# Kernel tuning notes

Measured on AMD Instinct MI355X. Metric: run time of the kernel, lower is better.

## Reference

```python
import jax, jax.numpy as jnp
import numpy as np

SIGMA1 = 1.0        # RBF bandwidth for kernel1
DYADIC_ORDER = 1    # dyadic grid refinement
LAMBD = 1.0         # ridge regularizer
INPUT_SCALE = 0.1   # keep signature-kernel values in fp32 range


def rbf_gram(X, Y, sigma):
    # X: (N,S,D), Y: (M,T,D) -> (N,M,S,T), sigkernel RBFKernel: exp(-||x-y||^2 / sigma)
    x2 = jnp.sum(X * X, axis=-1)  # (N,S)
    y2 = jnp.sum(Y * Y, axis=-1)  # (M,T)
    xy = jnp.einsum('nsd,mtd->nmst', X, Y)
    d2 = x2[:, None, :, None] + y2[None, :, None, :] - 2.0 * xy
    return jnp.exp(-d2 / sigma)


def linear_gram(X, Y):
    # sigkernel LinearKernel: inner product Gram
    return jnp.einsum('nsd,mtd->nmst', X, Y)


def sig_kernel_gram(G, dyadic_order):
    """Solve the Goursat PDE for the signature kernel on a dyadic grid.

    G: (N,M,S,T) static-kernel Gram. Returns (N,M) signature-kernel Gram.
    Update (sigkernel explicit scheme):
      k[i+1,j+1] = (k[i+1,j] + k[i,j+1]) * (1 + inc/2 + inc^2/12)
                   - k[i,j] * (1 - inc^2/12)
    """
    N, M, S, T = G.shape
    # double increments of the static kernel
    inc = G[:, :, 1:, 1:] - G[:, :, 1:, :-1] - G[:, :, :-1, 1:] + G[:, :, :-1, :-1]
    f = 2 ** dyadic_order
    inc = jnp.repeat(jnp.repeat(inc, f, axis=2), f, axis=3) / float(f * f)
    B = N * M
    P, Q = (S - 1) * f, (T - 1) * f
    inc = inc.reshape(B, P, Q)
    C1 = 1.0 + 0.5 * inc + inc * inc * (1.0 / 12.0)
    C2 = 1.0 - inc * inc * (1.0 / 12.0)
    ones_b = jnp.ones((B,), G.dtype)

    def row_step(prev_row, coeffs):
        c1, c2 = coeffs  # (B,Q) each

        def col_step(left, v):
            c1j, c2j, pj, pjm1 = v  # each (B,)
            new = (left + pj) * c1j - pjm1 * c2j
            return new, new

        xs = (c1.T, c2.T, prev_row[:, 1:].T, prev_row[:, :-1].T)  # (Q,B)
        _, vals = jax.lax.scan(col_step, ones_b, xs)  # (Q,B)
        new_row = jnp.concatenate([ones_b[:, None], vals.T], axis=1)  # (B,Q+1)
        return new_row, None

    row0 = jnp.ones((B, Q + 1), G.dtype)
    last_row, _ = jax.lax.scan(row_step, row0, (jnp.moveaxis(C1, 1, 0), jnp.moveaxis(C2, 1, 0)))
    return last_row[:, -1].reshape(N, M)


def cmmd(x, y, z):
    N = x.shape[0]
    K = sig_kernel_gram(rbf_gram(x, x, SIGMA1), DYADIC_ORDER)
    L_gen = sig_kernel_gram(linear_gram(y, y), DYADIC_ORDER)
    L_true = sig_kernel_gram(linear_gram(z, z), DYADIC_ORDER)
    L_mix = sig_kernel_gram(linear_gram(y, z), DYADIC_ORDER)
    Ktildeinv = jnp.linalg.inv(K + jnp.eye(N, dtype=K.dtype) * LAMBD)
    A = K @ Ktildeinv  # shared left factor

    def tr(L):
        return jnp.trace(A @ (L @ Ktildeinv))

    return tr(L_gen) + tr(L_true) - 2.0 * tr(L_mix)


def setup_inputs() -> dict:
    key = jax.random.key(0)
    k1, k2, k3 = jax.random.split(key, 3)
    shape = (64, 33, 8)
    return {
        'x': jax.random.normal(k1, shape, dtype=jnp.float32) * INPUT_SCALE,
        'y': jax.random.normal(k2, shape, dtype=jnp.float32) * INPUT_SCALE,
        'z': jax.random.normal(k3, shape, dtype=jnp.float32) * INPUT_SCALE,
    }


def reference(x, y, z):
    return cmmd(x, y, z)
```

## Files before the change

### kernel.cpp

```cpp
#include <hip/hip_runtime.h>
#include <hip/hip_fp16.h>
#include <math.h>


#define SLEN 33

__device__ __forceinline__ float rl(float v, int lane) {
    return __int_as_float(__builtin_amdgcn_readlane(__float_as_int(v), lane));
}

__global__ __launch_bounds__(64, 5)
void sigker_pde_kernel(const float* __restrict__ x,
                       const float* __restrict__ y,
                       const float* __restrict__ z,
                       float* __restrict__ ws) {
    __shared__ float4 Xi4[2][66];
    __shared__ __half incH[2][1024];

    const int lane = threadIdx.x;
    const int h = lane >> 5;
    const int p = lane & 31;

    int b = blockIdx.x, g, loc;
    if (b < 1040)      { g = 0; loc = b; }
    else if (b < 2080) { g = 1; loc = b - 1040; }
    else if (b < 3120) { g = 2; loc = b - 2080; }
    else               { g = 3; loc = b - 3120; }

    int pair = 2 * loc + h, gi, gj;
    if (g == 3) {
        gi = pair >> 6; gj = pair & 63;
    } else {
        float ff = sqrtf(8.0f * (float)pair + 1.0f);
        gi = (int)((ff - 1.0f) * 0.5f);
        while ((gi + 1) * (gi + 2) / 2 <= pair) ++gi;
        while (gi * (gi + 1) / 2 > pair) --gi;
        gj = pair - gi * (gi + 1) / 2;
    }

    const float* Ap = (g == 0) ? x : ((g == 2) ? z : y);
    const float* Bp = (g == 0) ? x : ((g == 1) ? y : z);
    const float4* As = (const float4*)(Ap + gi * (SLEN * 8));
    const float4* Bs = (const float4*)(Bp + gj * (SLEN * 8));

    for (int k = p; k < 66; k += 32) Xi4[h][k] = As[k];
    float4 b0 = Bs[2*p],   b1 = Bs[2*p+1];
    float4 b2 = Bs[2*p+2], b3 = Bs[2*p+3];
    __syncthreads();

    if (g == 0) {
        float nprev;
        {
            float4 a0 = Xi4[h][0], a1 = Xi4[h][1];
            float d0=a0.x-b0.x,d1=a0.y-b0.y,d2=a0.z-b0.z,d3=a0.w-b0.w;
            float d4=a1.x-b1.x,d5=a1.y-b1.y,d6=a1.z-b1.z,d7=a1.w-b1.w;
            float da = d0*d0+d1*d1+d2*d2+d3*d3+d4*d4+d5*d5+d6*d6+d7*d7;
            float e0=a0.x-b2.x,e1=a0.y-b2.y,e2=a0.z-b2.z,e3=a0.w-b2.w;
            float e4=a1.x-b3.x,e5=a1.y-b3.y,e6=a1.z-b3.z,e7=a1.w-b3.w;
            float db = e0*e0+e1*e1+e2*e2+e3*e3+e4*e4+e5*e5+e6*e6+e7*e7;
            nprev = __expf(-db) - __expf(-da);
        }
        for (int k = 1; k <= 32; ++k) {
            float4 a0 = Xi4[h][2*k], a1 = Xi4[h][2*k+1];
            float d0=a0.x-b0.x,d1=a0.y-b0.y,d2=a0.z-b0.z,d3=a0.w-b0.w;
            float d4=a1.x-b1.x,d5=a1.y-b1.y,d6=a1.z-b1.z,d7=a1.w-b1.w;
            float da = d0*d0+d1*d1+d2*d2+d3*d3+d4*d4+d5*d5+d6*d6+d7*d7;
            float e0=a0.x-b2.x,e1=a0.y-b2.y,e2=a0.z-b2.z,e3=a0.w-b2.w;
            float e4=a1.x-b3.x,e5=a1.y-b3.y,e6=a1.z-b3.z,e7=a1.w-b3.w;
            float db = e0*e0+e1*e1+e2*e2+e3*e3+e4*e4+e5*e5+e6*e6+e7*e7;
            float diffk = __expf(-db) - __expf(-da);
            incH[h][(k-1)*32 + p] = __float2half(0.25f * (diffk - nprev));
            nprev = diffk;
        }
    } else {
        float e0=b2.x-b0.x, e1=b2.y-b0.y, e2=b2.z-b0.z, e3=b2.w-b0.w;
        float e4=b3.x-b1.x, e5=b3.y-b1.y, e6=b3.z-b1.z, e7=b3.w-b1.w;
        float4 a0 = Xi4[h][0], a1 = Xi4[h][1];
        #pragma unroll 4
        for (int k = 0; k < 32; ++k) {
            float4 a2 = Xi4[h][2*k+2], a3 = Xi4[h][2*k+3];
            float acc = (a2.x-a0.x)*e0 + (a2.y-a0.y)*e1
                      + (a2.z-a0.z)*e2 + (a2.w-a0.w)*e3
                      + (a3.x-a1.x)*e4 + (a3.y-a1.y)*e5
                      + (a3.z-a1.z)*e6 + (a3.w-a1.w)*e7;
            incH[h][k*32 + p] = __float2half(0.25f * acc);
            a0 = a2; a1 = a3;
        }
    }
    __syncthreads();

    float c01 = 1.0f, c10 = 1.0f, c11 = 1.0f, dcarry = 1.0f;
    const bool isrow0 = (p == 0);
    const __half* incrow = &incH[h][p * 32];
    #pragma unroll 4
    for (int m = 0; m < 63; ++m) {
        float nb10 = __shfl_up(c10, 1);
        float nb11 = __shfl_up(c11, 1);
        int t = m - p;
        float incv = __half2float(incrow[t & 31]);
        float n0 = isrow0 ? 1.0f : nb10;
        float n1 = isrow0 ? 1.0f : nb11;
        bool t0 = (t == 0);
        float w0 = t0 ? 1.0f : c01;
        float w1 = t0 ? 1.0f : c11;
        float d  = t0 ? 1.0f : dcarry;
        float i2 = incv * incv * (1.0f / 12.0f);
        float C1 = 1.0f + 0.5f * incv + i2;
        float C2 = 1.0f - i2;
        float v00 = (w0  + n0 ) * C1 - d   * C2;
        float v01 = (v00 + n1 ) * C1 - n0  * C2;
        float v10 = (v00 + w1 ) * C1 - w0  * C2;
        float v11 = (v10 + v01) * C1 - v00 * C2;
        c01 = v01; c10 = v10; c11 = v11;
        dcarry = n1;
    }

    if (p == 31) {
        float* dst = ws + g * 4096;
        dst[gi * 64 + gj] = c11;
        if (g != 3) dst[gj * 64 + gi] = c11;
    }
}

__global__ __launch_bounds__(1024, 1)
void gj_trace_kernel(const float* __restrict__ ws, float* __restrict__ out) {
    __shared__ float prow[2][2][64];
    __shared__ float Kls[64 * 65];
    __shared__ float red[16];

    const int tid = threadIdx.x;
    const int c = tid & 63, w = tid >> 6;
    const float* K  = ws;
    const float* Lg = ws + 4096;
    const float* Lt = ws + 8192;
    const float* Lm = ws + 12288;

    float m[4];
    #pragma unroll
    for (int i = 0; i < 4; ++i) {
        int r = w * 4 + i;
        m[i] = K[r * 64 + c] + ((r == c) ? 1.0f : 0.0f);
    }

    #pragma unroll
    for (int rnd = 0; rnd < 32; ++rnd) {
        const int p0 = 2 * rnd, p1 = p0 + 1;
        const int wp = p0 >> 2;
        const int i0 = p0 & 3, i1 = i0 + 1;
        const int buf = rnd & 1;
        if (w == wp) {
            float a  = rl(m[i0], p0), bq = rl(m[i0], p1);
            float cq = rl(m[i1], p0), dq = rl(m[i1], p1);
            float dinv = 1.0f / (a * dq - bq * cq);
            float P00 =  dq * dinv, P01 = -bq * dinv;
            float P10 = -cq * dinv, P11 =  a  * dinv;
            float sp0 = P00 * m[i0] + P01 * m[i1];
            float sp1 = P10 * m[i0] + P11 * m[i1];
            sp0 = (c == p0) ? P00 : ((c == p1) ? P01 : sp0);
            sp1 = (c == p0) ? P10 : ((c == p1) ? P11 : sp1);
            m[i0] = sp0; m[i1] = sp1;
            prow[buf][0][c] = sp0;
            prow[buf][1][c] = sp1;
        }
        __syncthreads();
        float s0 = prow[buf][0][c],  s1 = prow[buf][1][c];
        float q00 = prow[buf][0][p0], q01 = prow[buf][0][p1];
        float q10 = prow[buf][1][p0], q11 = prow[buf][1][p1];
        #pragma unroll
        for (int i = 0; i < 4; ++i) {
            bool pivotRow = (w == wp) && (i == i0 || i == i1);
            float f0 = rl(m[i], p0);
            float f1 = rl(m[i], p1);
            float nv = m[i] - f0 * s0 - f1 * s1;
            float wb0 = -(f0 * q00 + f1 * q10);
            float wb1 = -(f0 * q01 + f1 * q11);
            nv = (c == p0) ? wb0 : ((c == p1) ? wb1 : nv);
            if (!pivotRow) m[i] = nv;
        }
    }

    #pragma unroll
    for (int i = 0; i < 4; ++i)
        Kls[(w * 4 + i) * 65 + c] = m[i];
    __syncthreads();

    float acc[4] = {0.0f, 0.0f, 0.0f, 0.0f};
    #pragma unroll 4
    for (int k = 0; k < 64; ++k) {
        float rv = Kls[k * 65 + c];
        #pragma unroll
        for (int i = 0; i < 4; ++i)
            acc[i] = fmaf(rl(m[i], k), rv, acc[i]);
    }

    float local = 0.0f;
    #pragma unroll
    for (int i = 0; i < 4; ++i) {
        int r = w * 4 + i;
        float lc = Lg[r * 64 + c] + Lt[r * 64 + c] - 2.0f * Lm[r * 64 + c];
        local += (m[i] - acc[i]) * lc;
    }
    #pragma unroll
    for (int off = 32; off > 0; off >>= 1)
        local += __shfl_down(local, off);
    if (c == 0) red[w] = local;
    __syncthreads();
    if (tid == 0) {
        float v = 0.0f;
        #pragma unroll
        for (int i = 0; i < 16; ++i) v += red[i];
        out[0] = v;
    }
}

extern "C" void kernel_launch(void* const* d_in, const int* in_sizes, int n_in,
                              void* d_out, int out_size, void* d_ws, size_t ws_size,
                              hipStream_t stream) {
    const float* x = (const float*)d_in[0];
    const float* y = (const float*)d_in[1];
    const float* z = (const float*)d_in[2];
    float* out = (float*)d_out;
    float* ws  = (float*)d_ws;

    sigker_pde_kernel<<<5168, 64, 0, stream>>>(x, y, z, ws);
    gj_trace_kernel<<<1, 1024, 0, stream>>>(ws, out);
}
```

Before: 105.4 us.

## Map each lane to two PDE rows and pack four pairs per wavefront

The PDE kernel now gives each lane a 2-row strip of the 64x64 dyadic grid, so 16 lanes serve one pair and a 64-lane block handles four pairs. Increments are stored as packed half2 values, one per row pair. The wavefront sweep shortens from 63 to 47 steps, and the block count halves. The intent is to cut shuffle-serialized anti-diagonal steps and raise work per wave, at the cost of more registers (launch bounds lowered to 3) and a longer dependent chain per step. The Gauss-Jordan loop is also switched to a non-unrolled form with runtime row selection to shrink code size.

```diff
diff --git a/kernel.cpp b/kernel.cpp
--- a/kernel.cpp
+++ b/kernel.cpp
@@ -9,25 +9,25 @@
     return __int_as_float(__builtin_amdgcn_readlane(__float_as_int(v), lane));
 }
 
-__global__ __launch_bounds__(64, 5)
+__global__ __launch_bounds__(64, 3)
 void sigker_pde_kernel(const float* __restrict__ x,
                        const float* __restrict__ y,
                        const float* __restrict__ z,
                        float* __restrict__ ws) {
-    __shared__ float4 Xi4[2][66];
-    __shared__ __half incH[2][1024];
+    __shared__ float4 XiS[4][66];
+    __shared__ __half2 inc2[4 * 520];
 
     const int lane = threadIdx.x;
-    const int h = lane >> 5;
-    const int p = lane & 31;
+    const int qt = lane >> 4;
+    const int s  = lane & 15;
 
     int b = blockIdx.x, g, loc;
-    if (b < 1040)      { g = 0; loc = b; }
-    else if (b < 2080) { g = 1; loc = b - 1040; }
-    else if (b < 3120) { g = 2; loc = b - 2080; }
-    else               { g = 3; loc = b - 3120; }
-
-    int pair = 2 * loc + h, gi, gj;
+    if (b < 520)       { g = 0; loc = b; }
+    else if (b < 1040) { g = 1; loc = b - 520; }
+    else if (b < 1560) { g = 2; loc = b - 1040; }
+    else               { g = 3; loc = b - 1560; }
+
+    int pair = 4 * loc + qt, gi, gj;
     if (g == 3) {
         gi = pair >> 6; gj = pair & 63;
     } else {
@@ -43,82 +43,122 @@
     const float4* As = (const float4*)(Ap + gi * (SLEN * 8));
     const float4* Bs = (const float4*)(Bp + gj * (SLEN * 8));
 
-    for (int k = p; k < 66; k += 32) Xi4[h][k] = As[k];
-    float4 b0 = Bs[2*p],   b1 = Bs[2*p+1];
-    float4 b2 = Bs[2*p+2], b3 = Bs[2*p+3];
-    __syncthreads();
+    for (int k = s; k < 66; k += 16) XiS[qt][k] = As[k];
+    float4 q0 = Bs[4*s],   q1 = Bs[4*s+1], q2 = Bs[4*s+2],
+           q3 = Bs[4*s+3], q4 = Bs[4*s+4], q5 = Bs[4*s+5];
+    __syncthreads();
+
+    __half2* incw = inc2 + qt * 520;
 
     if (g == 0) {
-        float nprev;
+        float p0g, p1g, p2g;
         {
-            float4 a0 = Xi4[h][0], a1 = Xi4[h][1];
-            float d0=a0.x-b0.x,d1=a0.y-b0.y,d2=a0.z-b0.z,d3=a0.w-b0.w;
-            float d4=a1.x-b1.x,d5=a1.y-b1.y,d6=a1.z-b1.z,d7=a1.w-b1.w;
-            float da = d0*d0+d1*d1+d2*d2+d3*d3+d4*d4+d5*d5+d6*d6+d7*d7;
-            float e0=a0.x-b2.x,e1=a0.y-b2.y,e2=a0.z-b2.z,e3=a0.w-b2.w;
-            float e4=a1.x-b3.x,e5=a1.y-b3.y,e6=a1.z-b3.z,e7=a1.w-b3.w;
-            float db = e0*e0+e1*e1+e2*e2+e3*e3+e4*e4+e5*e5+e6*e6+e7*e7;
-            nprev = __expf(-db) - __expf(-da);
-        }
-        for (int k = 1; k <= 32; ++k) {
-            float4 a0 = Xi4[h][2*k], a1 = Xi4[h][2*k+1];
-            float d0=a0.x-b0.x,d1=a0.y-b0.y,d2=a0.z-b0.z,d3=a0.w-b0.w;
-            float d4=a1.x-b1.x,d5=a1.y-b1.y,d6=a1.z-b1.z,d7=a1.w-b1.w;
-            float da = d0*d0+d1*d1+d2*d2+d3*d3+d4*d4+d5*d5+d6*d6+d7*d7;
-            float e0=a0.x-b2.x,e1=a0.y-b2.y,e2=a0.z-b2.z,e3=a0.w-b2.w;
-            float e4=a1.x-b3.x,e5=a1.y-b3.y,e6=a1.z-b3.z,e7=a1.w-b3.w;
-            float db = e0*e0+e1*e1+e2*e2+e3*e3+e4*e4+e5*e5+e6*e6+e7*e7;
-            float diffk = __expf(-db) - __expf(-da);
-            incH[h][(k-1)*32 + p] = __float2half(0.25f * (diffk - nprev));
-            nprev = diffk;
+            float4 a0 = XiS[qt][0], a1 = XiS[qt][1];
+            float u0=a0.x-q0.x,u1=a0.y-q0.y,u2=a0.z-q0.z,u3=a0.w-q0.w;
+            float u4=a1.x-q1.x,u5=a1.y-q1.y,u6=a1.z-q1.z,u7=a1.w-q1.w;
+            p0g = __expf(-(u0*u0+u1*u1+u2*u2+u3*u3+u4*u4+u5*u5+u6*u6+u7*u7));
+            float v0=a0.x-q2.x,v1=a0.y-q2.y,v2=a0.z-q2.z,v3=a0.w-q2.w;
+            float v4=a1.x-q3.x,v5=a1.y-q3.y,v6=a1.z-q3.z,v7=a1.w-q3.w;
+            p1g = __expf(-(v0*v0+v1*v1+v2*v2+v3*v3+v4*v4+v5*v5+v6*v6+v7*v7));
+            float w0=a0.x-q4.x,w1=a0.y-q4.y,w2=a0.z-q4.z,w3=a0.w-q4.w;
+            float w4=a1.x-q5.x,w5=a1.y-q5.y,w6=a1.z-q5.z,w7=a1.w-q5.w;
+            p2g = __expf(-(w0*w0+w1*w1+w2*w2+w3*w3+w4*w4+w5*w5+w6*w6+w7*w7));
+        }
+        float t00 = 0.0f, t01 = 0.0f;
+        #pragma unroll 2
+        for (int r = 1; r <= 32; ++r) {
+            float4 a0 = XiS[qt][2*r], a1 = XiS[qt][2*r+1];
+            float u0=a0.x-q0.x,u1=a0.y-q0.y,u2=a0.z-q0.z,u3=a0.w-q0.w;
+            float u4=a1.x-q1.x,u5=a1.y-q1.y,u6=a1.z-q1.z,u7=a1.w-q1.w;
+            float c0g = __expf(-(u0*u0+u1*u1+u2*u2+u3*u3+u4*u4+u5*u5+u6*u6+u7*u7));
+            float v0=a0.x-q2.x,v1=a0.y-q2.y,v2=a0.z-q2.z,v3=a0.w-q2.w;
+            float v4=a1.x-q3.x,v5=a1.y-q3.y,v6=a1.z-q3.z,v7=a1.w-q3.w;
+            float c1g = __expf(-(v0*v0+v1*v1+v2*v2+v3*v3+v4*v4+v5*v5+v6*v6+v7*v7));
+            float w0=a0.x-q4.x,w1=a0.y-q4.y,w2=a0.z-q4.z,w3=a0.w-q4.w;
+            float w4=a1.x-q5.x,w5=a1.y-q5.y,w6=a1.z-q5.z,w7=a1.w-q5.w;
+            float c2g = __expf(-(w0*w0+w1*w1+w2*w2+w3*w3+w4*w4+w5*w5+w6*w6+w7*w7));
+            int rr = r - 1;
+            float iA = 0.25f * ((c1g - c0g) - (p1g - p0g));
+            float iB = 0.25f * ((c2g - c1g) - (p2g - p1g));
+            if ((rr & 1) == 0) { t00 = iA; t01 = iB; }
+            else {
+                int sp = rr >> 1;
+                incw[sp * 32 + 2*s]     = __halves2half2(__float2half(t00), __float2half(iA));
+                incw[sp * 32 + 2*s + 1] = __halves2half2(__float2half(t01), __float2half(iB));
+            }
+            p0g = c0g; p1g = c1g; p2g = c2g;
         }
     } else {
-        float e0=b2.x-b0.x, e1=b2.y-b0.y, e2=b2.z-b0.z, e3=b2.w-b0.w;
-        float e4=b3.x-b1.x, e5=b3.y-b1.y, e6=b3.z-b1.z, e7=b3.w-b1.w;
-        float4 a0 = Xi4[h][0], a1 = Xi4[h][1];
-        #pragma unroll 4
-        for (int k = 0; k < 32; ++k) {
-            float4 a2 = Xi4[h][2*k+2], a3 = Xi4[h][2*k+3];
-            float acc = (a2.x-a0.x)*e0 + (a2.y-a0.y)*e1
-                      + (a2.z-a0.z)*e2 + (a2.w-a0.w)*e3
-                      + (a3.x-a1.x)*e4 + (a3.y-a1.y)*e5
-                      + (a3.z-a1.z)*e6 + (a3.w-a1.w)*e7;
-            incH[h][k*32 + p] = __float2half(0.25f * acc);
-            a0 = a2; a1 = a3;
-        }
-    }
-    __syncthreads();
-
-    float c01 = 1.0f, c10 = 1.0f, c11 = 1.0f, dcarry = 1.0f;
-    const bool isrow0 = (p == 0);
-    const __half* incrow = &incH[h][p * 32];
-    #pragma unroll 4
-    for (int m = 0; m < 63; ++m) {
-        float nb10 = __shfl_up(c10, 1);
-        float nb11 = __shfl_up(c11, 1);
-        int t = m - p;
-        float incv = __half2float(incrow[t & 31]);
-        float n0 = isrow0 ? 1.0f : nb10;
-        float n1 = isrow0 ? 1.0f : nb11;
+        float e0=(q2.x-q0.x)*0.25f, e1=(q2.y-q0.y)*0.25f,
+              e2=(q2.z-q0.z)*0.25f, e3=(q2.w-q0.w)*0.25f,
+              e4=(q3.x-q1.x)*0.25f, e5=(q3.y-q1.y)*0.25f,
+              e6=(q3.z-q1.z)*0.25f, e7=(q3.w-q1.w)*0.25f;
+        float f0=(q4.x-q2.x)*0.25f, f1=(q4.y-q2.y)*0.25f,
+              f2=(q4.z-q2.z)*0.25f, f3=(q4.w-q2.w)*0.25f,
+              f4=(q5.x-q3.x)*0.25f, f5=(q5.y-q3.y)*0.25f,
+              f6=(q5.z-q3.z)*0.25f, f7=(q5.w-q3.w)*0.25f;
+        float4 a0 = XiS[qt][0], a1 = XiS[qt][1];
+        #pragma unroll 2
+        for (int sp = 0; sp < 16; ++sp) {
+            float4 a2 = XiS[qt][4*sp+2], a3 = XiS[qt][4*sp+3];
+            float4 a4 = XiS[qt][4*sp+4], a5 = XiS[qt][4*sp+5];
+            float d0=a2.x-a0.x, d1=a2.y-a0.y, d2=a2.z-a0.z, d3=a2.w-a0.w;
+            float d4=a3.x-a1.x, d5=a3.y-a1.y, d6=a3.z-a1.z, d7=a3.w-a1.w;
+            float g0v=a4.x-a2.x, g1v=a4.y-a2.y, g2v=a4.z-a2.z, g3v=a4.w-a2.w;
+            float g4v=a5.x-a3.x, g5v=a5.y-a3.y, g6v=a5.z-a3.z, g7v=a5.w-a3.w;
+            float i00 = d0*e0+d1*e1+d2*e2+d3*e3+d4*e4+d5*e5+d6*e6+d7*e7;
+            float i01 = d0*f0+d1*f1+d2*f2+d3*f3+d4*f4+d5*f5+d6*f6+d7*f7;
+            float i10 = g0v*e0+g1v*e1+g2v*e2+g3v*e3+g4v*e4+g5v*e5+g6v*e6+g7v*e7;
+            float i11 = g0v*f0+g1v*f1+g2v*f2+g3v*f3+g4v*f4+g5v*f5+g6v*f6+g7v*f7;
+            incw[sp * 32 + 2*s]     = __halves2half2(__float2half(i00), __float2half(i10));
+            incw[sp * 32 + 2*s + 1] = __halves2half2(__float2half(i01), __float2half(i11));
+            a0 = a4; a1 = a5;
+        }
+    }
+    __syncthreads();
+
+    float cA01 = 1.0f, cA11 = 1.0f, dA = 1.0f;
+    float cB01 = 1.0f, cB10 = 1.0f, cB11 = 1.0f;
+    const bool stop = (s == 0);
+    const __half2* incr = incw + s * 32;
+    #pragma unroll 2
+    for (int m = 0; m < 47; ++m) {
+        float nb0 = __shfl_up(cB10, 1);
+        float nb1 = __shfl_up(cB11, 1);
+        int t = m - s;
+        __half2 hv = incr[t & 31];
+        float incA = __low2float(hv), incB = __high2float(hv);
+        float nA0 = stop ? 1.0f : nb0;
+        float nA1 = stop ? 1.0f : nb1;
         bool t0 = (t == 0);
-        float w0 = t0 ? 1.0f : c01;
-        float w1 = t0 ? 1.0f : c11;
-        float d  = t0 ? 1.0f : dcarry;
-        float i2 = incv * incv * (1.0f / 12.0f);
-        float C1 = 1.0f + 0.5f * incv + i2;
-        float C2 = 1.0f - i2;
-        float v00 = (w0  + n0 ) * C1 - d   * C2;
-        float v01 = (v00 + n1 ) * C1 - n0  * C2;
-        float v10 = (v00 + w1 ) * C1 - w0  * C2;
-        float v11 = (v10 + v01) * C1 - v00 * C2;
-        c01 = v01; c10 = v10; c11 = v11;
-        dcarry = n1;
-    }
-
-    if (p == 31) {
+        float wA0 = t0 ? 1.0f : cA01;
+        float wA1 = t0 ? 1.0f : cA11;
+        float dAx = t0 ? 1.0f : dA;
+        float wB0 = t0 ? 1.0f : cB01;
+        float wB1 = t0 ? 1.0f : cB11;
+        float dBx = t0 ? 1.0f : cA11;
+        float iA = incA * incA * (1.0f / 12.0f);
+        float C1A = 1.0f + 0.5f * incA + iA;
+        float C2A = 1.0f - iA;
+        float iB = incB * incB * (1.0f / 12.0f);
+        float C1B = 1.0f + 0.5f * incB + iB;
+        float C2B = 1.0f - iB;
+        float vA00 = (wA0 + nA0 ) * C1A - dAx * C2A;
+        float vA01 = (vA00 + nA1 ) * C1A - nA0 * C2A;
+        float vA10 = (vA00 + wA1 ) * C1A - wA0 * C2A;
+        float vA11 = (vA10 + vA01) * C1A - vA00 * C2A;
+        float vB00 = (wB0 + vA10) * C1B - dBx * C2B;
+        float vB01 = (vB00 + vA11) * C1B - vA10 * C2B;
+        float vB10 = (vB00 + wB1 ) * C1B - wB0 * C2B;
+        float vB11 = (vB10 + vB01) * C1B - vB00 * C2B;
+        cA01 = vA01; cA11 = vA11; dA = nA1;
+        cB01 = vB01; cB10 = vB10; cB11 = vB11;
+    }
+
+    if (s == 15) {
         float* dst = ws + g * 4096;
-        dst[gi * 64 + gj] = c11;
-        if (g != 3) dst[gj * 64 + gi] = c11;
+        dst[gi * 64 + gj] = cB11;
+        if (g != 3) dst[gj * 64 + gi] = cB11;
     }
 }
 
@@ -142,23 +182,25 @@
         m[i] = K[r * 64 + c] + ((r == c) ? 1.0f : 0.0f);
     }
 
-    #pragma unroll
+    #pragma unroll 1
     for (int rnd = 0; rnd < 32; ++rnd) {
         const int p0 = 2 * rnd, p1 = p0 + 1;
-        const int wp = p0 >> 2;
-        const int i0 = p0 & 3, i1 = i0 + 1;
+        const int wp = rnd >> 1;
+        const bool hi = (rnd & 1);
         const int buf = rnd & 1;
         if (w == wp) {
-            float a  = rl(m[i0], p0), bq = rl(m[i0], p1);
-            float cq = rl(m[i1], p0), dq = rl(m[i1], p1);
+            float x0 = hi ? m[2] : m[0];
+            float x1 = hi ? m[3] : m[1];
+            float a  = rl(x0, p0), bq = rl(x0, p1);
+            float cq = rl(x1, p0), dq = rl(x1, p1);
             float dinv = 1.0f / (a * dq - bq * cq);
             float P00 =  dq * dinv, P01 = -bq * dinv;
             float P10 = -cq * dinv, P11 =  a  * dinv;
-            float sp0 = P00 * m[i0] + P01 * m[i1];
-            float sp1 = P10 * m[i0] + P11 * m[i1];
+            float sp0 = P00 * x0 + P01 * x1;
+            float sp1 = P10 * x0 + P11 * x1;
             sp0 = (c == p0) ? P00 : ((c == p1) ? P01 : sp0);
             sp1 = (c == p0) ? P10 : ((c == p1) ? P11 : sp1);
-            m[i0] = sp0; m[i1] = sp1;
+            if (hi) { m[2] = sp0; m[3] = sp1; } else { m[0] = sp0; m[1] = sp1; }
             prow[buf][0][c] = sp0;
             prow[buf][1][c] = sp1;
         }
@@ -166,9 +208,10 @@
         float s0 = prow[buf][0][c],  s1 = prow[buf][1][c];
         float q00 = prow[buf][0][p0], q01 = prow[buf][0][p1];
         float q10 = prow[buf][1][p0], q11 = prow[buf][1][p1];
+        const int i0 = hi ? 2 : 0;
         #pragma unroll
         for (int i = 0; i < 4; ++i) {
-            bool pivotRow = (w == wp) && (i == i0 || i == i1);
+            bool pivotRow = (w == wp) && (i == i0 || i == i0 + 1);
             float f0 = rl(m[i], p0);
             float f1 = rl(m[i], p1);
             float nv = m[i] - f0 * s0 - f1 * s1;
@@ -222,6 +265,6 @@
     float* out = (float*)d_out;
     float* ws  = (float*)d_ws;
 
-    sigker_pde_kernel<<<5168, 64, 0, stream>>>(x, y, z, ws);
+    sigker_pde_kernel<<<2584, 64, 0, stream>>>(x, y, z, ws);
     gj_trace_kernel<<<1, 1024, 0, stream>>>(ws, out);
 }
```

Result: no change. 107.0 us (+1.5%).

## Fold L-combination into Gauss-Jordan sweep to drop trailing matmul

Applied to the files above, without the earlier changes.

Appends the combined L matrix (Lg + Lt - 2Lm) as extra right-hand-side columns of the in-register Gauss-Jordan inversion, so the same sweep yields Ktilde^-1 L. The trace is then taken as tr(Kinv L) minus the elementwise product of Kinv and Kinv L, using A = I - Kinv. This removes the shared-memory staging and the 64x64 matrix product that followed the inversion. In exchange each elimination round does more register work and more shared-memory traffic, and the round loop is now only partly unrolled, which could add loop overhead.

```diff
diff --git a/kernel.cpp b/kernel.cpp
--- a/kernel.cpp
+++ b/kernel.cpp
@@ -124,8 +124,7 @@
 
 __global__ __launch_bounds__(1024, 1)
 void gj_trace_kernel(const float* __restrict__ ws, float* __restrict__ out) {
-    __shared__ float prow[2][2][64];
-    __shared__ float Kls[64 * 65];
+    __shared__ float prow[2][4][64];
     __shared__ float red[16];
 
     const int tid = threadIdx.x;
@@ -135,70 +134,70 @@
     const float* Lt = ws + 8192;
     const float* Lm = ws + 12288;
 
-    float m[4];
+    float m[4], mL[4];
     #pragma unroll
     for (int i = 0; i < 4; ++i) {
         int r = w * 4 + i;
-        m[i] = K[r * 64 + c] + ((r == c) ? 1.0f : 0.0f);
-    }
-
-    #pragma unroll
-    for (int rnd = 0; rnd < 32; ++rnd) {
-        const int p0 = 2 * rnd, p1 = p0 + 1;
-        const int wp = p0 >> 2;
-        const int i0 = p0 & 3, i1 = i0 + 1;
-        const int buf = rnd & 1;
-        if (w == wp) {
-            float a  = rl(m[i0], p0), bq = rl(m[i0], p1);
-            float cq = rl(m[i1], p0), dq = rl(m[i1], p1);
-            float dinv = 1.0f / (a * dq - bq * cq);
-            float P00 =  dq * dinv, P01 = -bq * dinv;
-            float P10 = -cq * dinv, P11 =  a  * dinv;
-            float sp0 = P00 * m[i0] + P01 * m[i1];
-            float sp1 = P10 * m[i0] + P11 * m[i1];
-            sp0 = (c == p0) ? P00 : ((c == p1) ? P01 : sp0);
-            sp1 = (c == p0) ? P10 : ((c == p1) ? P11 : sp1);
-            m[i0] = sp0; m[i1] = sp1;
-            prow[buf][0][c] = sp0;
-            prow[buf][1][c] = sp1;
-        }
-        __syncthreads();
-        float s0 = prow[buf][0][c],  s1 = prow[buf][1][c];
-        float q00 = prow[buf][0][p0], q01 = prow[buf][0][p1];
-        float q10 = prow[buf][1][p0], q11 = prow[buf][1][p1];
+        m[i]  = K[r * 64 + c] + ((r == c) ? 1.0f : 0.0f);
+        mL[i] = Lg[r * 64 + c] + Lt[r * 64 + c] - 2.0f * Lm[r * 64 + c];
+    }
+
+    #pragma unroll 1
+    for (int it = 0; it < 8; ++it) {
+        const int base = 8 * it;
         #pragma unroll
-        for (int i = 0; i < 4; ++i) {
-            bool pivotRow = (w == wp) && (i == i0 || i == i1);
-            float f0 = rl(m[i], p0);
-            float f1 = rl(m[i], p1);
-            float nv = m[i] - f0 * s0 - f1 * s1;
-            float wb0 = -(f0 * q00 + f1 * q10);
-            float wb1 = -(f0 * q01 + f1 * q11);
-            nv = (c == p0) ? wb0 : ((c == p1) ? wb1 : nv);
-            if (!pivotRow) m[i] = nv;
-        }
-    }
-
-    #pragma unroll
-    for (int i = 0; i < 4; ++i)
-        Kls[(w * 4 + i) * 65 + c] = m[i];
-    __syncthreads();
-
-    float acc[4] = {0.0f, 0.0f, 0.0f, 0.0f};
-    #pragma unroll 4
-    for (int k = 0; k < 64; ++k) {
-        float rv = Kls[k * 65 + c];
-        #pragma unroll
-        for (int i = 0; i < 4; ++i)
-            acc[i] = fmaf(rl(m[i], k), rv, acc[i]);
+        for (int j = 0; j < 4; ++j) {
+            const int p0 = base + 2 * j, p1 = p0 + 1;
+            const int i0 = (2 * j) & 3, i1 = i0 + 1;
+            const int buf = j & 1;
+            const int wp = 2 * it + (j >> 1);
+            if (w == wp) {
+                float x0 = m[i0], x1 = m[i1];
+                float xL0 = mL[i0], xL1 = mL[i1];
+                float a  = rl(x0, p0), bq = rl(x0, p1);
+                float cq = rl(x1, p0), dq = rl(x1, p1);
+                float dinv = 1.0f / (a * dq - bq * cq);
+                float P00 =  dq * dinv, P01 = -bq * dinv;
+                float P10 = -cq * dinv, P11 =  a  * dinv;
+                float sp0 = P00 * x0 + P01 * x1;
+                float sp1 = P10 * x0 + P11 * x1;
+                sp0 = (c == p0) ? P00 : ((c == p1) ? P01 : sp0);
+                sp1 = (c == p0) ? P10 : ((c == p1) ? P11 : sp1);
+                float sL0 = P00 * xL0 + P01 * xL1;
+                float sL1 = P10 * xL0 + P11 * xL1;
+                m[i0] = sp0;  m[i1] = sp1;
+                mL[i0] = sL0; mL[i1] = sL1;
+                prow[buf][0][c] = sp0;
+                prow[buf][1][c] = sp1;
+                prow[buf][2][c] = sL0;
+                prow[buf][3][c] = sL1;
+            }
+            __syncthreads();
+            float s0  = prow[buf][0][c],  s1  = prow[buf][1][c];
+            float sL0 = prow[buf][2][c],  sL1 = prow[buf][3][c];
+            float q00 = prow[buf][0][p0], q01 = prow[buf][0][p1];
+            float q10 = prow[buf][1][p0], q11 = prow[buf][1][p1];
+            #pragma unroll
+            for (int i = 0; i < 4; ++i) {
+                bool pivotRow = (w == wp) && (i == i0 || i == i1);
+                float f0 = rl(m[i], p0);
+                float f1 = rl(m[i], p1);
+                float nv = m[i] - f0 * s0 - f1 * s1;
+                float wb0 = -(f0 * q00 + f1 * q10);
+                float wb1 = -(f0 * q01 + f1 * q11);
+                nv = (c == p0) ? wb0 : ((c == p1) ? wb1 : nv);
+                float nL = mL[i] - f0 * sL0 - f1 * sL1;
+                if (!pivotRow) { m[i] = nv; mL[i] = nL; }
+            }
+        }
     }
 
     float local = 0.0f;
     #pragma unroll
     for (int i = 0; i < 4; ++i) {
         int r = w * 4 + i;
-        float lc = Lg[r * 64 + c] + Lt[r * 64 + c] - 2.0f * Lm[r * 64 + c];
-        local += (m[i] - acc[i]) * lc;
+        float diag = (r == c) ? mL[i] : 0.0f;
+        local += diag - m[i] * mL[i];
     }
     #pragma unroll
     for (int off = 32; off > 0; off >>= 1)
```

Result: slower. 108.2 us (+2.7%).
